# Performance work log

Hardware: AMD Instinct MI355X
Metric: run time of the kernel (lower is better)

Reference implementation:

```python
import jax, jax.numpy as jnp
import numpy as np

B, T, HID = 2, 2048, 1024
NH, HD = 16, 64          # attn_heads, head_size (NH*HD == HID)
FF = 4 * HID
LN_EPS = 1e-5            # torch nn.LayerNorm default


def setup_inputs() -> dict:
    key = jax.random.key(0)
    ks = jax.random.split(key, 14)
    s = lambda fan_in: fan_in ** -0.5
    return {
        "embedding": jax.random.normal(ks[0], (B, T, HID), jnp.float32),
        # per-head q/k/v projections stacked: [HID, NH, HD] (no bias, as in torch code)
        "Wq": jax.random.normal(ks[1], (HID, NH, HD), jnp.float32) * s(HID),
        "Wk": jax.random.normal(ks[2], (HID, NH, HD), jnp.float32) * s(HID),
        "Wv": jax.random.normal(ks[3], (HID, NH, HD), jnp.float32) * s(HID),
        "Wo": jax.random.normal(ks[4], (HID, HID), jnp.float32) * s(HID),
        "W1": jax.random.normal(ks[5], (HID, FF), jnp.float32) * s(HID),
        "b1": jnp.zeros((FF,), jnp.float32),
        "W2": jax.random.normal(ks[6], (FF, HID), jnp.float32) * s(FF),
        "b2": jnp.zeros((HID,), jnp.float32),
        "g1": jnp.ones((HID,), jnp.float32),
        "be1": jnp.zeros((HID,), jnp.float32),
        "g2": jnp.ones((HID,), jnp.float32),
        "be2": jnp.zeros((HID,), jnp.float32),
    }


def _layer_norm(h, g, b):
    mu = jnp.mean(h, axis=-1, keepdims=True)
    var = jnp.mean(jnp.square(h - mu), axis=-1, keepdims=True)
    return (h - mu) * jax.lax.rsqrt(var + LN_EPS) * g + b


def _block(x, Wq, Wk, Wv, Wo, W1, b1, W2, b2, g1, be1, g2, be2):
    # --- causal multi-head self-attention (pre-LN) ---
    h = _layer_norm(x, g1, be1)
    q = jnp.einsum('btd,dhk->bhtk', h, Wq)
    k = jnp.einsum('btd,dhk->bhtk', h, Wk)
    v = jnp.einsum('btd,dhk->bhtk', h, Wv)
    scores = jnp.einsum('bhtk,bhsk->bhts', q, k) * (HD ** -0.5)
    causal = jnp.tril(jnp.ones((T, T), bool))
    scores = jnp.where(causal, scores, -jnp.inf)
    attn = jax.nn.softmax(scores, axis=-1)
    ctx = jnp.einsum('bhts,bhsk->bhtk', attn, v)          # [B,NH,T,HD]
    ctx = ctx.transpose(0, 2, 1, 3).reshape(x.shape[0], x.shape[1], HID)
    x = x + ctx @ Wo
    # --- feed-forward (pre-LN) ---
    h2 = _layer_norm(x, g2, be2)
    ff = jax.nn.relu(h2 @ W1 + b1) @ W2 + b2
    return x + ff


def reference(embedding, Wq, Wk, Wv, Wo, W1, b1, W2, b2, g1, be1, g2, be2):
    return _block(embedding, Wq, Wk, Wv, Wo, W1, b1, W2, b2, g1, be1, g2, be2)
```

## Files before the change

kernel.cpp:

```cpp
#include <hip/hip_runtime.h>
#include <math.h>

#define HIDDEN 1024
#define SEQ    2048
#define NHEAD  16
#define HDIM   64
#define ROWS   (2 * SEQ)

typedef float  floatx4  __attribute__((ext_vector_type(4)));
typedef float  floatx16 __attribute__((ext_vector_type(16)));
typedef __bf16 bf16x8   __attribute__((ext_vector_type(8)));
typedef __bf16 bf16x4   __attribute__((ext_vector_type(4)));

#define AS1(p) ((const __attribute__((address_space(1))) void*)(p))
#define AS3(p) ((__attribute__((address_space(3))) void*)(p))

#define SWZ(row, chunk) ((((chunk) ^ ((row) & 7)) * 8))

__global__ __launch_bounds__(256) void prep_all(const float* __restrict__ Wq,
                                                const float* __restrict__ Wk,
                                                const float* __restrict__ Wv,
                                                const float* __restrict__ Wo,
                                                const float* __restrict__ W1,
                                                const float* __restrict__ W2,
                                                __bf16* __restrict__ BtQKV,
                                                __bf16* __restrict__ BtO,
                                                __bf16* __restrict__ Bt1,
                                                __bf16* __restrict__ Bt2,
                                                const float* __restrict__ emb,
                                                const float* __restrict__ g1,
                                                const float* __restrict__ be1,
                                                __bf16* __restrict__ h) {
    int id = blockIdx.x;
    int tid = threadIdx.x;
    if (id >= 12288) {
        int row = id - 12288;
        const float* xr = emb + (size_t)row * HIDDEN;
        float4 v = *(const float4*)(xr + tid * 4);
        float s  = v.x + v.y + v.z + v.w;
        float s2 = v.x * v.x + v.y * v.y + v.z * v.z + v.w * v.w;
#pragma unroll
        for (int off = 1; off < 64; off <<= 1) {
            s  += __shfl_xor(s, off, 64);
            s2 += __shfl_xor(s2, off, 64);
        }
        __shared__ float red[8];
        int wid = tid >> 6;
        if ((tid & 63) == 0) { red[wid] = s; red[wid + 4] = s2; }
        __syncthreads();
        s  = red[0] + red[1] + red[2] + red[3];
        s2 = red[4] + red[5] + red[6] + red[7];
        float mu  = s * (1.0f / HIDDEN);
        float var = fmaxf(s2 * (1.0f / HIDDEN) - mu * mu, 0.0f);
        float inv = rsqrtf(var + 1e-5f);
        float4 gv = *(const float4*)(g1 + tid * 4);
        float4 bv = *(const float4*)(be1 + tid * 4);
        bf16x4 o;
        o[0] = (__bf16)((v.x - mu) * inv * gv.x + bv.x);
        o[1] = (__bf16)((v.y - mu) * inv * gv.y + bv.y);
        o[2] = (__bf16)((v.z - mu) * inv * gv.z + bv.z);
        o[3] = (__bf16)((v.w - mu) * inv * gv.w + bv.w);
        *(bf16x4*)(h + (size_t)row * HIDDEN + tid * 4) = o;
        return;
    }
    __shared__ float t[32][33];
    const float* in; __bf16* out; int K, N, nt, kt;
    if (id < 4096) {
        int job = id >> 10, tt = id & 1023;
        nt = tt & 31; kt = tt >> 5; K = 1024; N = 1024;
        if (job == 0)      { in = Wq; out = BtQKV; }
        else if (job == 1) { in = Wk; out = BtQKV + 1024 * 1024; }
        else if (job == 2) { in = Wv; out = BtQKV + 2 * 1024 * 1024; }
        else               { in = Wo; out = BtO; }
    } else if (id < 8192) {
        int tt = id - 4096;
        nt = tt & 127; kt = tt >> 7; K = 1024; N = 4096; in = W1; out = Bt1;
    } else {
        int tt = id - 8192;
        nt = tt & 31; kt = tt >> 5; K = 4096; N = 1024; in = W2; out = Bt2;
    }
    int n0 = nt * 32, k0 = kt * 32;
    int r  = tid >> 3;
    int c4 = (tid & 7) * 4;
    float4 v = *(const float4*)(in + (size_t)(k0 + r) * N + n0 + c4);
    t[r][c4 + 0] = v.x; t[r][c4 + 1] = v.y; t[r][c4 + 2] = v.z; t[r][c4 + 3] = v.w;
    __syncthreads();
    bf16x4 o;
    o[0] = (__bf16)t[c4 + 0][r];
    o[1] = (__bf16)t[c4 + 1][r];
    o[2] = (__bf16)t[c4 + 2][r];
    o[3] = (__bf16)t[c4 + 3][r];
    *(bf16x4*)(out + (size_t)(n0 + r) * K + k0 + c4) = o;
}

__global__ __launch_bounds__(256) void red_wo_ln(const float* __restrict__ emb,
                                                 const __bf16* __restrict__ p0,
                                                 const __bf16* __restrict__ p1,
                                                 const float* __restrict__ g,
                                                 const float* __restrict__ beta,
                                                 float* __restrict__ out,
                                                 __bf16* __restrict__ h2) {
    int row = blockIdx.x;
    int tid = threadIdx.x;
    size_t i = (size_t)row * HIDDEN + tid * 4;
    float4 e = *(const float4*)(emb + i);
    bf16x4 a = *(const bf16x4*)(p0 + i);
    bf16x4 b = *(const bf16x4*)(p1 + i);
    float4 v;
    v.x = e.x + (float)a[0] + (float)b[0];
    v.y = e.y + (float)a[1] + (float)b[1];
    v.z = e.z + (float)a[2] + (float)b[2];
    v.w = e.w + (float)a[3] + (float)b[3];
    *(float4*)(out + i) = v;

    float s  = v.x + v.y + v.z + v.w;
    float s2 = v.x * v.x + v.y * v.y + v.z * v.z + v.w * v.w;
#pragma unroll
    for (int off = 1; off < 64; off <<= 1) {
        s  += __shfl_xor(s, off, 64);
        s2 += __shfl_xor(s2, off, 64);
    }
    __shared__ float red[8];
    int wid = tid >> 6;
    if ((tid & 63) == 0) { red[wid] = s; red[wid + 4] = s2; }
    __syncthreads();
    s  = red[0] + red[1] + red[2] + red[3];
    s2 = red[4] + red[5] + red[6] + red[7];
    float mu  = s * (1.0f / HIDDEN);
    float var = fmaxf(s2 * (1.0f / HIDDEN) - mu * mu, 0.0f);
    float inv = rsqrtf(var + 1e-5f);
    float4 gv = *(const float4*)(g + tid * 4);
    float4 bv = *(const float4*)(beta + tid * 4);
    bf16x4 o;
    o[0] = (__bf16)((v.x - mu) * inv * gv.x + bv.x);
    o[1] = (__bf16)((v.y - mu) * inv * gv.y + bv.y);
    o[2] = (__bf16)((v.z - mu) * inv * gv.z + bv.z);
    o[3] = (__bf16)((v.w - mu) * inv * gv.w + bv.w);
    *(bf16x4*)(h2 + i) = o;
}

__device__ __forceinline__ void mfma_core128(const __bf16* __restrict__ A,
                                             const __bf16* __restrict__ Bt,
                                             int Kstride, int Klen,
                                             int m0, int n0, int tid,
                                             floatx16 (&acc)[2][2]) {
    __shared__ __bf16 As[2 * 128 * 32];
    __shared__ __bf16 Bs[2 * 128 * 32];
    const int BUF = 128 * 32;
    int lane = tid & 63;
    int wave = tid >> 6;
    int wr = wave >> 1, wc = wave & 1;

    int sr = lane >> 2;
    int sk = 8 * ((lane & 3) ^ ((sr >> 1) & 3));
    const __bf16* ga0 = A  + (size_t)(m0 + wave * 16 + sr) * Kstride + sk;
    const __bf16* ga1 = ga0 + (size_t)64 * Kstride;
    const __bf16* gb0 = Bt + (size_t)(n0 + wave * 16 + sr) * Kstride + sk;
    const __bf16* gb1 = gb0 + (size_t)64 * Kstride;
    __bf16* la0 = &As[wave * 512];
    __bf16* la1 = &As[2048 + wave * 512];
    __bf16* lb0 = &Bs[wave * 512];
    __bf16* lb1 = &Bs[2048 + wave * 512];

    int fm = lane & 31;
    int gswz = (lane >> 1) & 3;
    int slot0 = ((lane >> 5) + 0) ^ gswz;
    int slot1 = ((lane >> 5) + 2) ^ gswz;

    __builtin_amdgcn_global_load_lds(AS1(ga0), AS3(la0), 16, 0, 0);
    __builtin_amdgcn_global_load_lds(AS1(ga1), AS3(la1), 16, 0, 0);
    __builtin_amdgcn_global_load_lds(AS1(gb0), AS3(lb0), 16, 0, 0);
    __builtin_amdgcn_global_load_lds(AS1(gb1), AS3(lb1), 16, 0, 0);

    int buf = 0;
    for (int k0 = 0; k0 < Klen; k0 += 32, buf ^= 1) {
        __syncthreads();
        if (k0 + 32 < Klen) {
            int nb = (buf ^ 1) * BUF;
            __builtin_amdgcn_global_load_lds(AS1(ga0 + k0 + 32), AS3(la0 + nb), 16, 0, 0);
            __builtin_amdgcn_global_load_lds(AS1(ga1 + k0 + 32), AS3(la1 + nb), 16, 0, 0);
            __builtin_amdgcn_global_load_lds(AS1(gb0 + k0 + 32), AS3(lb0 + nb), 16, 0, 0);
            __builtin_amdgcn_global_load_lds(AS1(gb1 + k0 + 32), AS3(lb1 + nb), 16, 0, 0);
        }
        const __bf16* Ab = As + buf * BUF;
        const __bf16* Bb = Bs + buf * BUF;

        bf16x8 af[2][2], bfv[2][2];
#pragma unroll
        for (int i = 0; i < 2; i++) {
            const __bf16* rp = Ab + (size_t)(wr * 64 + i * 32 + fm) * 32;
            af[i][0] = *(const bf16x8*)(rp + slot0 * 8);
            af[i][1] = *(const bf16x8*)(rp + slot1 * 8);
        }
#pragma unroll
        for (int j = 0; j < 2; j++) {
            const __bf16* rp = Bb + (size_t)(wc * 64 + j * 32 + fm) * 32;
            bfv[j][0] = *(const bf16x8*)(rp + slot0 * 8);
            bfv[j][1] = *(const bf16x8*)(rp + slot1 * 8);
        }
#pragma unroll
        for (int t = 0; t < 2; t++)
#pragma unroll
            for (int i = 0; i < 2; i++)
#pragma unroll
                for (int j = 0; j < 2; j++)
                    acc[i][j] = __builtin_amdgcn_mfma_f32_32x32x16_bf16(
                        af[i][t], bfv[j][t], acc[i][j], 0, 0, 0);
    }
}

template <typename OutT, bool BIAS, bool RELU, bool RES>
__global__ __launch_bounds__(256) void mgemm(const __bf16* __restrict__ A,
                                             const __bf16* __restrict__ Bt,
                                             const float* __restrict__ bias,
                                             const float* __restrict__ res,
                                             OutT* __restrict__ C,
                                             int M, int N, int Kstride, int Klen) {
    int tid = threadIdx.x;
    int lane = tid & 63;
    int wave = tid >> 6;
    int m0 = blockIdx.x * 128, n0 = blockIdx.y * 128;
    int wr = wave >> 1, wc = wave & 1;
    floatx16 acc[2][2] = {};
    mfma_core128(A, Bt, Kstride, Klen, m0, n0, tid, acc);

#pragma unroll
    for (int i = 0; i < 2; i++) {
#pragma unroll
        for (int j = 0; j < 2; j++) {
            int col  = n0 + wc * 64 + j * 32 + (lane & 31);
            int rowb = m0 + wr * 64 + i * 32 + 4 * (lane >> 5);
#pragma unroll
            for (int reg = 0; reg < 16; reg++) {
                int row = rowb + (reg & 3) + 8 * (reg >> 2);
                float v = acc[i][j][reg];
                if (BIAS) v += bias[col];
                if (RELU) v = fmaxf(v, 0.0f);
                if (RES)  v += res[(size_t)row * N + col];
                C[(size_t)row * N + col] = (OutT)v;
            }
        }
    }
}

__global__ __launch_bounds__(256) void mgemm_qkv(const __bf16* __restrict__ A,
                                                 const __bf16* __restrict__ Bt,
                                                 __bf16* __restrict__ C,
                                                 __bf16* __restrict__ Vt) {
    const int N = 3072;
    int tid = threadIdx.x;
    int lane = tid & 63;
    int wave = tid >> 6;
    int m0 = blockIdx.x * 128, n0 = blockIdx.y * 128;
    int wr = wave >> 1, wc = wave & 1;
    floatx16 acc[2][2] = {};
    mfma_core128(A, Bt, 1024, 1024, m0, n0, tid, acc);

#pragma unroll
    for (int i = 0; i < 2; i++) {
#pragma unroll
        for (int j = 0; j < 2; j++) {
            int col  = n0 + wc * 64 + j * 32 + (lane & 31);
            int rowb = m0 + wr * 64 + i * 32 + 4 * (lane >> 5);
            if (col < 2048) {
#pragma unroll
                for (int reg = 0; reg < 16; reg++) {
                    int row = rowb + (reg & 3) + 8 * (reg >> 2);
                    C[(size_t)row * N + col] = (__bf16)acc[i][j][reg];
                }
            } else {
                int vcol = col - 2048;
                int hh = vcol >> 6, dd = vcol & 63;
#pragma unroll
                for (int rq = 0; rq < 4; rq++) {
                    int row0 = rowb + 8 * rq;
                    int bb = row0 >> 11;
                    int tt = row0 & 2047;
                    bf16x4 pack;
                    pack[0] = (__bf16)acc[i][j][4 * rq + 0];
                    pack[1] = (__bf16)acc[i][j][4 * rq + 1];
                    pack[2] = (__bf16)acc[i][j][4 * rq + 2];
                    pack[3] = (__bf16)acc[i][j][4 * rq + 3];
                    *(bf16x4*)&Vt[(((size_t)bb * 16 + hh) * 64 + dd) * SEQ + tt] = pack;
                }
            }
        }
    }
}

__global__ __launch_bounds__(256) void mgemm_sk(const __bf16* __restrict__ A,
                                                const __bf16* __restrict__ Bt,
                                                __bf16* __restrict__ P0,
                                                __bf16* __restrict__ P3,
                                                int M, int N, int Kstride, int Klen) {
    int z = blockIdx.z;
    const __bf16* Az  = A  + (size_t)z * Klen;
    const __bf16* Btz = Bt + (size_t)z * Klen;
    __bf16* C = (z == 3) ? P3 : (P0 + (size_t)z * M * N);

    int tid = threadIdx.x;
    int lane = tid & 63;
    int wave = tid >> 6;
    int m0 = blockIdx.x * 128, n0 = blockIdx.y * 128;
    int wr = wave >> 1, wc = wave & 1;
    floatx16 acc[2][2] = {};
    mfma_core128(Az, Btz, Kstride, Klen, m0, n0, tid, acc);

#pragma unroll
    for (int i = 0; i < 2; i++) {
#pragma unroll
        for (int j = 0; j < 2; j++) {
            int col  = n0 + wc * 64 + j * 32 + (lane & 31);
            int rowb = m0 + wr * 64 + i * 32 + 4 * (lane >> 5);
#pragma unroll
            for (int reg = 0; reg < 16; reg++) {
                int row = rowb + (reg & 3) + 8 * (reg >> 2);
                C[(size_t)row * N + col] = (__bf16)acc[i][j][reg];
            }
        }
    }
}

__global__ __launch_bounds__(256) void red_w2(const __bf16* __restrict__ p0,
                                              const __bf16* __restrict__ p3,
                                              const float* __restrict__ b2,
                                              float* __restrict__ out,
                                              int N) {
    size_t i = ((size_t)blockIdx.x * 256 + threadIdx.x) * 8;
    const size_t MN = (size_t)ROWS * HIDDEN;
    bf16x8 a = *(const bf16x8*)(p0 + i);
    bf16x8 b = *(const bf16x8*)(p0 + MN + i);
    bf16x8 c = *(const bf16x8*)(p0 + 2 * MN + i);
    bf16x8 d = *(const bf16x8*)(p3 + i);
    int col = (int)(i & (size_t)(N - 1));
    float4 bb0 = *(const float4*)(b2 + col);
    float4 bb1 = *(const float4*)(b2 + col + 4);
    float4 o0 = *(const float4*)(out + i);
    float4 o1 = *(const float4*)(out + i + 4);
    o0.x += (float)a[0] + (float)b[0] + (float)c[0] + (float)d[0] + bb0.x;
    o0.y += (float)a[1] + (float)b[1] + (float)c[1] + (float)d[1] + bb0.y;
    o0.z += (float)a[2] + (float)b[2] + (float)c[2] + (float)d[2] + bb0.z;
    o0.w += (float)a[3] + (float)b[3] + (float)c[3] + (float)d[3] + bb0.w;
    o1.x += (float)a[4] + (float)b[4] + (float)c[4] + (float)d[4] + bb1.x;
    o1.y += (float)a[5] + (float)b[5] + (float)c[5] + (float)d[5] + bb1.y;
    o1.z += (float)a[6] + (float)b[6] + (float)c[6] + (float)d[6] + bb1.z;
    o1.w += (float)a[7] + (float)b[7] + (float)c[7] + (float)d[7] + bb1.w;
    *(float4*)(out + i)     = o0;
    *(float4*)(out + i + 4) = o1;
}

__global__ __launch_bounds__(256) void attn_mfma(const __bf16* __restrict__ qkv,
                                                 const __bf16* __restrict__ Vt,
                                                 __bf16* __restrict__ ctx) {
    __shared__ __bf16 Ks[64 * 64];
    __shared__ __bf16 Vs[64 * 64];
    __shared__ __bf16 Ps[4][16 * 64];
    const int QKVW = 3 * HIDDEN;

    int bh = blockIdx.x;
    int qt = gridDim.y - 1 - blockIdx.y;
    int b = bh >> 4, h = bh & 15;
    int tid = threadIdx.x;
    int lane = tid & 63;
    int w = tid >> 6;
    int m = lane & 15;
    int g = lane >> 4;

    const float QSC = 1.44269504f / 8.0f;
    bf16x8 qf[2];
    {
        const __bf16* Qp = qkv + (size_t)(b * SEQ + qt * 64 + w * 16 + m) * QKVW
                         + h * HDIM + g * 8;
        qf[0] = *(const bf16x8*)(Qp);
        qf[1] = *(const bf16x8*)(Qp + 32);
#pragma unroll
        for (int t = 0; t < 2; t++)
#pragma unroll
            for (int i = 0; i < 8; i++)
                qf[t][i] = (__bf16)((float)qf[t][i] * QSC);
    }

    bf16x8 onesf;
#pragma unroll
    for (int i = 0; i < 8; i++) onesf[i] = (__bf16)1.0f;

    floatx4 oacc[4] = {};
    floatx4 lacc = {};

    int srow = tid >> 2;
    int sc0  = (tid & 3) * 2;
    const __bf16* Kg = qkv + (size_t)(b * SEQ) * QKVW + HIDDEN + h * HDIM;
    const __bf16* Vg = Vt + (size_t)bh * HDIM * SEQ;

    bf16x8 pk0, pk1, pv0, pv1;
    {
        const __bf16* kp = Kg + (size_t)srow * QKVW + sc0 * 8;
        pk0 = *(const bf16x8*)kp;
        pk1 = *(const bf16x8*)(kp + 8);
        const __bf16* vp = Vg + (size_t)srow * SEQ + sc0 * 8;
        pv0 = *(const bf16x8*)vp;
        pv1 = *(const bf16x8*)(vp + 8);
    }

    for (int kt = 0; kt <= qt; kt++) {
        __syncthreads();
        *(bf16x8*)&Ks[srow * 64 + SWZ(srow, sc0)]     = pk0;
        *(bf16x8*)&Ks[srow * 64 + SWZ(srow, sc0 + 1)] = pk1;
        *(bf16x8*)&Vs[srow * 64 + SWZ(srow, sc0)]     = pv0;
        *(bf16x8*)&Vs[srow * 64 + SWZ(srow, sc0 + 1)] = pv1;
        __syncthreads();

        if (kt < qt) {
            const __bf16* kp = Kg + (size_t)((kt + 1) * 64 + srow) * QKVW + sc0 * 8;
            pk0 = *(const bf16x8*)kp;
            pk1 = *(const bf16x8*)(kp + 8);
            const __bf16* vp = Vg + (size_t)srow * SEQ + (kt + 1) * 64 + sc0 * 8;
            pv0 = *(const bf16x8*)vp;
            pv1 = *(const bf16x8*)(vp + 8);
        }

        floatx4 sacc[4] = {};
#pragma unroll
        for (int j = 0; j < 4; j++) {
#pragma unroll
            for (int t = 0; t < 2; t++) {
                int kr = 16 * j + m;
                bf16x8 kf = *(const bf16x8*)&Ks[kr * 64 + SWZ(kr, g + 4 * t)];
                sacc[j] = __builtin_amdgcn_mfma_f32_16x16x32_bf16(
                    qf[t], kf, sacc[j], 0, 0, 0);
            }
        }

        if (kt == qt) {
            int qlocal = w * 16 + 4 * g;
#pragma unroll
            for (int j = 0; j < 4; j++)
#pragma unroll
                for (int r = 0; r < 4; r++)
                    if (16 * j + m > qlocal + r) sacc[j][r] = -INFINITY;
        }

        __bf16* Pw = &Ps[w][0];
#pragma unroll
        for (int j = 0; j < 4; j++)
#pragma unroll
            for (int r = 0; r < 4; r++) {
                float p = exp2f(sacc[j][r]);
                int row = 4 * g + r;
                int key = 16 * j + m;
                Pw[row * 64 + SWZ(row, key >> 3) + (key & 7)] = (__bf16)p;
            }

#pragma unroll
        for (int t = 0; t < 2; t++) {
            bf16x8 pf = *(const bf16x8*)&Pw[m * 64 + SWZ(m, g + 4 * t)];
            lacc = __builtin_amdgcn_mfma_f32_16x16x32_bf16(pf, onesf, lacc, 0, 0, 0);
#pragma unroll
            for (int jd = 0; jd < 4; jd++) {
                int vr = 16 * jd + m;
                bf16x8 vf = *(const bf16x8*)&Vs[vr * 64 + SWZ(vr, g + 4 * t)];
                oacc[jd] = __builtin_amdgcn_mfma_f32_16x16x32_bf16(
                    pf, vf, oacc[jd], 0, 0, 0);
            }
        }
    }

#pragma unroll
    for (int r = 0; r < 4; r++) {
        float invl = 1.0f / lacc[r];
        int row = qt * 64 + w * 16 + 4 * g + r;
        __bf16* cp = ctx + (size_t)(b * SEQ + row) * HIDDEN + h * HDIM;
#pragma unroll
        for (int jd = 0; jd < 4; jd++)
            cp[16 * jd + m] = (__bf16)(oacc[jd][r] * invl);
    }
}

extern "C" void kernel_launch(void* const* d_in, const int* in_sizes, int n_in,
                              void* d_out, int out_size, void* d_ws, size_t ws_size,
                              hipStream_t stream) {
    (void)in_sizes; (void)n_in; (void)out_size; (void)ws_size;
    const float* emb = (const float*)d_in[0];
    const float* Wq  = (const float*)d_in[1];
    const float* Wk  = (const float*)d_in[2];
    const float* Wv  = (const float*)d_in[3];
    const float* Wo  = (const float*)d_in[4];
    const float* W1  = (const float*)d_in[5];
    const float* b1  = (const float*)d_in[6];
    const float* W2  = (const float*)d_in[7];
    const float* b2  = (const float*)d_in[8];
    const float* g1  = (const float*)d_in[9];
    const float* be1 = (const float*)d_in[10];
    const float* g2  = (const float*)d_in[11];
    const float* be2 = (const float*)d_in[12];
    float* out = (float*)d_out;

    __bf16* wsb = (__bf16*)d_ws;
    const size_t ME = 1024 * 1024;
    __bf16* h     = wsb;
    __bf16* qkv   = wsb + 4 * ME;
    __bf16* ctx   = wsb;
    __bf16* ff1   = wsb;
    __bf16* h2    = wsb + 16 * ME;
    __bf16* BtQKV = wsb + 20 * ME;
    __bf16* BtO   = wsb + 23 * ME;
    __bf16* Bt1   = wsb + 24 * ME;
    __bf16* Bt2   = wsb + 28 * ME;
    __bf16* Vt    = wsb + 32 * ME;
    __bf16* woP   = wsb + 4 * ME;
    __bf16* w2P0  = wsb + 16 * ME;
    __bf16* w2P3  = wsb + 32 * ME;

    prep_all<<<16384, 256, 0, stream>>>(Wq, Wk, Wv, Wo, W1, W2,
                                        BtQKV, BtO, Bt1, Bt2,
                                        emb, g1, be1, h);

    mgemm_qkv<<<dim3(32, 24), 256, 0, stream>>>(h, BtQKV, qkv, Vt);

    attn_mfma<<<dim3(32, 32), 256, 0, stream>>>(qkv, Vt, ctx);

    mgemm_sk<<<dim3(32, 8, 2), 256, 0, stream>>>(
        ctx, BtO, woP, nullptr, ROWS, 1024, 1024, 512);
    red_wo_ln<<<ROWS, 256, 0, stream>>>(emb, woP, woP + 4 * ME, g2, be2, out, h2);

    mgemm<__bf16, true, true, false><<<dim3(32, 32), 256, 0, stream>>>(
        h2, Bt1, b1, nullptr, ff1, ROWS, 4096, 1024, 1024);

    mgemm_sk<<<dim3(32, 8, 4), 256, 0, stream>>>(
        ff1, Bt2, w2P0, w2P3, ROWS, 1024, 4096, 1024);
    red_w2<<<2048, 256, 0, stream>>>(w2P0, w2P3, b2, out, 1024);
}
```

Before: 345.1 us.

## Pre-tile weights into MFMA fragment layout and atomically accumulate split-K outputs

Weights are now written by the prep kernel in a fragment-blocked layout, so the GEMM core loads B operands straight into registers with register double-buffering instead of staging them through LDS. Split-K partial products are added into the fp32 output with float atomics rather than written as bf16 partials and summed by separate reduction kernels. The residual copy moves into the prep kernel and the b2 bias into the LayerNorm kernel. This removes the partial-buffer traffic and the red_w2 kernel, and halves LDS use. In exchange it adds atomic contention, makes the summation order nondeterministic, and raises register pressure from the held B fragments.

```diff
diff --git a/kernel.cpp b/kernel.cpp
--- a/kernel.cpp
+++ b/kernel.cpp
@@ -30,13 +30,15 @@
                                                 const float* __restrict__ emb,
                                                 const float* __restrict__ g1,
                                                 const float* __restrict__ be1,
-                                                __bf16* __restrict__ h) {
+                                                __bf16* __restrict__ h,
+                                                float* __restrict__ xout) {
     int id = blockIdx.x;
     int tid = threadIdx.x;
     if (id >= 12288) {
         int row = id - 12288;
-        const float* xr = emb + (size_t)row * HIDDEN;
-        float4 v = *(const float4*)(xr + tid * 4);
+        size_t i = (size_t)row * HIDDEN + tid * 4;
+        float4 v = *(const float4*)(emb + i);
+        *(float4*)(xout + i) = v;
         float s  = v.x + v.y + v.z + v.w;
         float s2 = v.x * v.x + v.y * v.y + v.z * v.z + v.w * v.w;
 #pragma unroll
@@ -60,7 +62,7 @@
         o[1] = (__bf16)((v.y - mu) * inv * gv.y + bv.y);
         o[2] = (__bf16)((v.z - mu) * inv * gv.z + bv.z);
         o[3] = (__bf16)((v.w - mu) * inv * gv.w + bv.w);
-        *(bf16x4*)(h + (size_t)row * HIDDEN + tid * 4) = o;
+        *(bf16x4*)(h + i) = o;
         return;
     }
     __shared__ float t[32][33];
@@ -90,29 +92,21 @@
     o[1] = (__bf16)t[c4 + 1][r];
     o[2] = (__bf16)t[c4 + 2][r];
     o[3] = (__bf16)t[c4 + 3][r];
-    *(bf16x4*)(out + (size_t)(n0 + r) * K + k0 + c4) = o;
-}
-
-__global__ __launch_bounds__(256) void red_wo_ln(const float* __restrict__ emb,
-                                                 const __bf16* __restrict__ p0,
-                                                 const __bf16* __restrict__ p1,
-                                                 const float* __restrict__ g,
-                                                 const float* __restrict__ beta,
-                                                 float* __restrict__ out,
-                                                 __bf16* __restrict__ h2) {
+    int n = n0 + r, k = k0 + c4;
+    size_t blk = (size_t)(n >> 5) * (K >> 4) + (k >> 4);
+    int ln = ((k >> 3) & 1) * 32 + (n & 31);
+    *(bf16x4*)(out + blk * 512 + ln * 8 + (k & 7)) = o;
+}
+
+__global__ __launch_bounds__(256) void red_ln(const float* __restrict__ b2,
+                                              const float* __restrict__ g,
+                                              const float* __restrict__ beta,
+                                              float* __restrict__ out,
+                                              __bf16* __restrict__ h2) {
     int row = blockIdx.x;
     int tid = threadIdx.x;
     size_t i = (size_t)row * HIDDEN + tid * 4;
-    float4 e = *(const float4*)(emb + i);
-    bf16x4 a = *(const bf16x4*)(p0 + i);
-    bf16x4 b = *(const bf16x4*)(p1 + i);
-    float4 v;
-    v.x = e.x + (float)a[0] + (float)b[0];
-    v.y = e.y + (float)a[1] + (float)b[1];
-    v.z = e.z + (float)a[2] + (float)b[2];
-    v.w = e.w + (float)a[3] + (float)b[3];
-    *(float4*)(out + i) = v;
-
+    float4 v = *(const float4*)(out + i);
     float s  = v.x + v.y + v.z + v.w;
     float s2 = v.x * v.x + v.y * v.y + v.z * v.z + v.w * v.w;
 #pragma unroll
@@ -137,15 +131,17 @@
     o[2] = (__bf16)((v.z - mu) * inv * gv.z + bv.z);
     o[3] = (__bf16)((v.w - mu) * inv * gv.w + bv.w);
     *(bf16x4*)(h2 + i) = o;
+    float4 bb = *(const float4*)(b2 + tid * 4);
+    v.x += bb.x; v.y += bb.y; v.z += bb.z; v.w += bb.w;
+    *(float4*)(out + i) = v;
 }
 
 __device__ __forceinline__ void mfma_core128(const __bf16* __restrict__ A,
-                                             const __bf16* __restrict__ Bt,
-                                             int Kstride, int Klen,
+                                             const __bf16* __restrict__ BtF,
+                                             int Kstride, int kbase, int Klen,
                                              int m0, int n0, int tid,
                                              floatx16 (&acc)[2][2]) {
     __shared__ __bf16 As[2 * 128 * 32];
-    __shared__ __bf16 Bs[2 * 128 * 32];
     const int BUF = 128 * 32;
     int lane = tid & 63;
     int wave = tid >> 6;
@@ -153,24 +149,29 @@
 
     int sr = lane >> 2;
     int sk = 8 * ((lane & 3) ^ ((sr >> 1) & 3));
-    const __bf16* ga0 = A  + (size_t)(m0 + wave * 16 + sr) * Kstride + sk;
+    const __bf16* ga0 = A + (size_t)(m0 + wave * 16 + sr) * Kstride + kbase + sk;
     const __bf16* ga1 = ga0 + (size_t)64 * Kstride;
-    const __bf16* gb0 = Bt + (size_t)(n0 + wave * 16 + sr) * Kstride + sk;
-    const __bf16* gb1 = gb0 + (size_t)64 * Kstride;
     __bf16* la0 = &As[wave * 512];
     __bf16* la1 = &As[2048 + wave * 512];
-    __bf16* lb0 = &Bs[wave * 512];
-    __bf16* lb1 = &Bs[2048 + wave * 512];
 
     int fm = lane & 31;
     int gswz = (lane >> 1) & 3;
     int slot0 = ((lane >> 5) + 0) ^ gswz;
     int slot1 = ((lane >> 5) + 2) ^ gswz;
 
+    const __bf16* bb = BtF + ((size_t)((n0 >> 5) + wc * 2) * (Kstride >> 4)) * 512
+                     + (size_t)lane * 8;
+    const size_t jstr = (size_t)(Kstride >> 4) * 512;
+    int ci0 = kbase >> 4;
+
     __builtin_amdgcn_global_load_lds(AS1(ga0), AS3(la0), 16, 0, 0);
     __builtin_amdgcn_global_load_lds(AS1(ga1), AS3(la1), 16, 0, 0);
-    __builtin_amdgcn_global_load_lds(AS1(gb0), AS3(lb0), 16, 0, 0);
-    __builtin_amdgcn_global_load_lds(AS1(gb1), AS3(lb1), 16, 0, 0);
+    bf16x8 bcur[2][2], bnxt[2][2];
+#pragma unroll
+    for (int j = 0; j < 2; j++)
+#pragma unroll
+        for (int t = 0; t < 2; t++)
+            bcur[j][t] = *(const bf16x8*)(bb + j * jstr + (size_t)(ci0 + t) * 512);
 
     int buf = 0;
     for (int k0 = 0; k0 < Klen; k0 += 32, buf ^= 1) {
@@ -179,13 +180,15 @@
             int nb = (buf ^ 1) * BUF;
             __builtin_amdgcn_global_load_lds(AS1(ga0 + k0 + 32), AS3(la0 + nb), 16, 0, 0);
             __builtin_amdgcn_global_load_lds(AS1(ga1 + k0 + 32), AS3(la1 + nb), 16, 0, 0);
-            __builtin_amdgcn_global_load_lds(AS1(gb0 + k0 + 32), AS3(lb0 + nb), 16, 0, 0);
-            __builtin_amdgcn_global_load_lds(AS1(gb1 + k0 + 32), AS3(lb1 + nb), 16, 0, 0);
+            int ci = ci0 + ((k0 + 32) >> 4);
+#pragma unroll
+            for (int j = 0; j < 2; j++)
+#pragma unroll
+                for (int t = 0; t < 2; t++)
+                    bnxt[j][t] = *(const bf16x8*)(bb + j * jstr + (size_t)(ci + t) * 512);
         }
         const __bf16* Ab = As + buf * BUF;
-        const __bf16* Bb = Bs + buf * BUF;
-
-        bf16x8 af[2][2], bfv[2][2];
+        bf16x8 af[2][2];
 #pragma unroll
         for (int i = 0; i < 2; i++) {
             const __bf16* rp = Ab + (size_t)(wr * 64 + i * 32 + fm) * 32;
@@ -193,36 +196,34 @@
             af[i][1] = *(const bf16x8*)(rp + slot1 * 8);
         }
 #pragma unroll
-        for (int j = 0; j < 2; j++) {
-            const __bf16* rp = Bb + (size_t)(wc * 64 + j * 32 + fm) * 32;
-            bfv[j][0] = *(const bf16x8*)(rp + slot0 * 8);
-            bfv[j][1] = *(const bf16x8*)(rp + slot1 * 8);
-        }
-#pragma unroll
         for (int t = 0; t < 2; t++)
 #pragma unroll
             for (int i = 0; i < 2; i++)
 #pragma unroll
                 for (int j = 0; j < 2; j++)
                     acc[i][j] = __builtin_amdgcn_mfma_f32_32x32x16_bf16(
-                        af[i][t], bfv[j][t], acc[i][j], 0, 0, 0);
-    }
-}
-
-template <typename OutT, bool BIAS, bool RELU, bool RES>
+                        af[i][t], bcur[j][t], acc[i][j], 0, 0, 0);
+#pragma unroll
+        for (int j = 0; j < 2; j++)
+#pragma unroll
+            for (int t = 0; t < 2; t++)
+                bcur[j][t] = bnxt[j][t];
+    }
+}
+
+template <typename OutT, bool BIAS, bool RELU>
 __global__ __launch_bounds__(256) void mgemm(const __bf16* __restrict__ A,
-                                             const __bf16* __restrict__ Bt,
+                                             const __bf16* __restrict__ BtF,
                                              const float* __restrict__ bias,
-                                             const float* __restrict__ res,
                                              OutT* __restrict__ C,
-                                             int M, int N, int Kstride, int Klen) {
+                                             int N, int Kstride, int Klen) {
     int tid = threadIdx.x;
     int lane = tid & 63;
     int wave = tid >> 6;
     int m0 = blockIdx.x * 128, n0 = blockIdx.y * 128;
     int wr = wave >> 1, wc = wave & 1;
     floatx16 acc[2][2] = {};
-    mfma_core128(A, Bt, Kstride, Klen, m0, n0, tid, acc);
+    mfma_core128(A, BtF, Kstride, 0, Klen, m0, n0, tid, acc);
 
 #pragma unroll
     for (int i = 0; i < 2; i++) {
@@ -236,7 +237,6 @@
                 float v = acc[i][j][reg];
                 if (BIAS) v += bias[col];
                 if (RELU) v = fmaxf(v, 0.0f);
-                if (RES)  v += res[(size_t)row * N + col];
                 C[(size_t)row * N + col] = (OutT)v;
             }
         }
@@ -244,7 +244,7 @@
 }
 
 __global__ __launch_bounds__(256) void mgemm_qkv(const __bf16* __restrict__ A,
-                                                 const __bf16* __restrict__ Bt,
+                                                 const __bf16* __restrict__ BtF,
                                                  __bf16* __restrict__ C,
                                                  __bf16* __restrict__ Vt) {
     const int N = 3072;
@@ -254,7 +254,7 @@
     int m0 = blockIdx.x * 128, n0 = blockIdx.y * 128;
     int wr = wave >> 1, wc = wave & 1;
     floatx16 acc[2][2] = {};
-    mfma_core128(A, Bt, 1024, 1024, m0, n0, tid, acc);
+    mfma_core128(A, BtF, 1024, 0, 1024, m0, n0, tid, acc);
 
 #pragma unroll
     for (int i = 0; i < 2; i++) {
@@ -288,23 +288,18 @@
     }
 }
 
-__global__ __launch_bounds__(256) void mgemm_sk(const __bf16* __restrict__ A,
-                                                const __bf16* __restrict__ Bt,
-                                                __bf16* __restrict__ P0,
-                                                __bf16* __restrict__ P3,
-                                                int M, int N, int Kstride, int Klen) {
+__global__ __launch_bounds__(256) void mgemm_ska(const __bf16* __restrict__ A,
+                                                 const __bf16* __restrict__ BtF,
+                                                 float* __restrict__ out,
+                                                 int N, int Kstride, int Klen) {
     int z = blockIdx.z;
-    const __bf16* Az  = A  + (size_t)z * Klen;
-    const __bf16* Btz = Bt + (size_t)z * Klen;
-    __bf16* C = (z == 3) ? P3 : (P0 + (size_t)z * M * N);
-
     int tid = threadIdx.x;
     int lane = tid & 63;
     int wave = tid >> 6;
     int m0 = blockIdx.x * 128, n0 = blockIdx.y * 128;
     int wr = wave >> 1, wc = wave & 1;
     floatx16 acc[2][2] = {};
-    mfma_core128(Az, Btz, Kstride, Klen, m0, n0, tid, acc);
+    mfma_core128(A, BtF, Kstride, z * Klen, Klen, m0, n0, tid, acc);
 
 #pragma unroll
     for (int i = 0; i < 2; i++) {
@@ -315,38 +310,10 @@
 #pragma unroll
             for (int reg = 0; reg < 16; reg++) {
                 int row = rowb + (reg & 3) + 8 * (reg >> 2);
-                C[(size_t)row * N + col] = (__bf16)acc[i][j][reg];
-            }
-        }
-    }
-}
-
-__global__ __launch_bounds__(256) void red_w2(const __bf16* __restrict__ p0,
-                                              const __bf16* __restrict__ p3,
-                                              const float* __restrict__ b2,
-                                              float* __restrict__ out,
-                                              int N) {
-    size_t i = ((size_t)blockIdx.x * 256 + threadIdx.x) * 8;
-    const size_t MN = (size_t)ROWS * HIDDEN;
-    bf16x8 a = *(const bf16x8*)(p0 + i);
-    bf16x8 b = *(const bf16x8*)(p0 + MN + i);
-    bf16x8 c = *(const bf16x8*)(p0 + 2 * MN + i);
-    bf16x8 d = *(const bf16x8*)(p3 + i);
-    int col = (int)(i & (size_t)(N - 1));
-    float4 bb0 = *(const float4*)(b2 + col);
-    float4 bb1 = *(const float4*)(b2 + col + 4);
-    float4 o0 = *(const float4*)(out + i);
-    float4 o1 = *(const float4*)(out + i + 4);
-    o0.x += (float)a[0] + (float)b[0] + (float)c[0] + (float)d[0] + bb0.x;
-    o0.y += (float)a[1] + (float)b[1] + (float)c[1] + (float)d[1] + bb0.y;
-    o0.z += (float)a[2] + (float)b[2] + (float)c[2] + (float)d[2] + bb0.z;
-    o0.w += (float)a[3] + (float)b[3] + (float)c[3] + (float)d[3] + bb0.w;
-    o1.x += (float)a[4] + (float)b[4] + (float)c[4] + (float)d[4] + bb1.x;
-    o1.y += (float)a[5] + (float)b[5] + (float)c[5] + (float)d[5] + bb1.y;
-    o1.z += (float)a[6] + (float)b[6] + (float)c[6] + (float)d[6] + bb1.z;
-    o1.w += (float)a[7] + (float)b[7] + (float)c[7] + (float)d[7] + bb1.w;
-    *(float4*)(out + i)     = o0;
-    *(float4*)(out + i + 4) = o1;
+                unsafeAtomicAdd(&out[(size_t)row * N + col], acc[i][j][reg]);
+            }
+        }
+    }
 }
 
 __global__ __launch_bounds__(256) void attn_mfma(const __bf16* __restrict__ qkv,
@@ -507,26 +474,23 @@
     __bf16* Bt1   = wsb + 24 * ME;
     __bf16* Bt2   = wsb + 28 * ME;
     __bf16* Vt    = wsb + 32 * ME;
-    __bf16* woP   = wsb + 4 * ME;
-    __bf16* w2P0  = wsb + 16 * ME;
-    __bf16* w2P3  = wsb + 32 * ME;
 
     prep_all<<<16384, 256, 0, stream>>>(Wq, Wk, Wv, Wo, W1, W2,
                                         BtQKV, BtO, Bt1, Bt2,
-                                        emb, g1, be1, h);
+                                        emb, g1, be1, h, out);
 
     mgemm_qkv<<<dim3(32, 24), 256, 0, stream>>>(h, BtQKV, qkv, Vt);
 
     attn_mfma<<<dim3(32, 32), 256, 0, stream>>>(qkv, Vt, ctx);
 
-    mgemm_sk<<<dim3(32, 8, 2), 256, 0, stream>>>(
-        ctx, BtO, woP, nullptr, ROWS, 1024, 1024, 512);
-    red_wo_ln<<<ROWS, 256, 0, stream>>>(emb, woP, woP + 4 * ME, g2, be2, out, h2);
-
-    mgemm<__bf16, true, true, false><<<dim3(32, 32), 256, 0, stream>>>(
-        h2, Bt1, b1, nullptr, ff1, ROWS, 4096, 1024, 1024);
-
-    mgemm_sk<<<dim3(32, 8, 4), 256, 0, stream>>>(
-        ff1, Bt2, w2P0, w2P3, ROWS, 1024, 4096, 1024);
-    red_w2<<<2048, 256, 0, stream>>>(w2P0, w2P3, b2, out, 1024);
-}
+    mgemm_ska<<<dim3(32, 8, 2), 256, 0, stream>>>(
+        ctx, BtO, out, 1024, 1024, 512);
+
+    red_ln<<<ROWS, 256, 0, stream>>>(b2, g2, be2, out, h2);
+
+    mgemm<__bf16, true, true><<<dim3(32, 32), 256, 0, stream>>>(
+        h2, Bt1, b1, ff1, 4096, 1024, 1024);
+
+    mgemm_ska<<<dim3(32, 8, 4), 256, 0, stream>>>(
+        ff1, Bt2, out, 1024, 4096, 1024);
+}
```

Result: slower. 369.4 us (+7.0%).
